# Performance work log

Hardware: AMD Instinct MI355X
Metric: run time of the kernel (lower is better)

The kernel has to match this reference:

```python
import jax, jax.numpy as jnp
import numpy as np
import math

# dims
B, L, D = 2, 2048, 1024          # batch, seq len, embedding_dim
HID, ATT, H = 1024, 512, 8       # linear_hidden_dim, attention_dim, num_heads
DQK, DUV = ATT // H, HID // H    # 64, 128
NBUCK = 64                       # time_num_buckets
MAX_SPAN = 86400 * 90            # max_time_span
EPS = 1e-6
OUT_DIM = 2 * HID + 2 * ATT      # uvqk output dim = 3072


def _time_boundaries():
    # RelativeAttentionBiasModule._build_boundaries: pure log buckets
    steps = NBUCK - 1
    log_part = np.exp(np.linspace(0.0, math.log(MAX_SPAN), steps))
    b = np.unique(np.floor(np.clip(log_part, 1, None)).astype(np.int64)).astype(np.float32)
    return jnp.asarray(b)

_BOUNDARIES = _time_boundaries()  # len <= 63, indices < NBUCK


def setup_inputs() -> dict:
    key = jax.random.key(0)
    ks = jax.random.split(key, 8)
    x = jax.random.normal(ks[0], (B, L, D), dtype=jnp.float32)
    timestamps = jnp.sort(
        jax.random.randint(ks[1], (B, L), 0, 2592000), axis=-1
    )  # chronological event times (seconds)
    attn_mask = jnp.tril(jnp.ones((L, L), dtype=bool))[None].repeat(B, axis=0)  # causal
    W_uvqk = jax.random.normal(ks[2], (OUT_DIM, D), dtype=jnp.float32) * 0.02
    b_uvqk = jnp.zeros((OUT_DIM,), dtype=jnp.float32)
    time_bias = jax.random.normal(ks[3], (NBUCK, H), dtype=jnp.float32) * 0.02
    W_o = jax.random.normal(ks[4], (D, HID), dtype=jnp.float32) * 0.02
    b_o = jnp.zeros((D,), dtype=jnp.float32)
    rms_w = jnp.ones((HID,), dtype=jnp.float32)
    return {"x": x, "timestamps": timestamps, "attn_mask": attn_mask,
            "W_uvqk": W_uvqk, "b_uvqk": b_uvqk, "time_bias": time_bias,
            "W_o": W_o, "b_o": b_o, "rms_w": rms_w}


def reference(x, timestamps, attn_mask, W_uvqk, b_uvqk, time_bias, W_o, b_o, rms_w):
    Bx, Lx, _ = x.shape
    scale = 1.0 / math.sqrt(DQK)

    # fused uvqk projection + act1 (silu)
    h = jax.nn.silu(x @ W_uvqk.T + b_uvqk)  # [B, L, OUT_DIM]
    u, v, q, k = jnp.split(h, [HID, 2 * HID, 2 * HID + ATT], axis=-1)

    def heads(t, d):  # [B, L, H*d] -> [B, H, L, d]
        return t.reshape(Bx, Lx, H, d).transpose(0, 2, 1, 3)

    u = heads(u, DUV)
    v = heads(v, DUV)
    q = heads(q, DQK) * scale
    k = heads(k, DQK)

    logits = jnp.einsum('bhid,bhjd->bhij', q.astype(jnp.float32), k.astype(jnp.float32))

    # bucketized relative-time bias (per-head)
    tdiff = jnp.abs(timestamps[:, :, None] - timestamps[:, None, :])
    tdiff = jnp.clip(tdiff, 1, None).astype(jnp.float32)  # clamp_min(1)
    bk = jnp.searchsorted(_BOUNDARIES, tdiff, side='left')  # torch.bucketize right=False
    rab = time_bias[bk].transpose(0, 3, 1, 2)  # [B, H, L, L]

    # pointwise silu attention (no softmax), masked
    A = jax.nn.silu(logits + rab) * attn_mask[:, None].astype(jnp.float32)

    y = jnp.einsum('bhij,bhjd->bhid', A, v)               # [B, H, L, DUV]
    y = y.transpose(0, 2, 1, 3).reshape(Bx, Lx, HID)       # merge heads
    u_m = u.transpose(0, 2, 1, 3).reshape(Bx, Lx, HID)

    # RMSNorm then U-gate
    rms = y * jax.lax.rsqrt(jnp.mean(y * y, axis=-1, keepdims=True) + EPS) * rms_w
    y_point = rms.astype(x.dtype) * u_m

    return y_point @ W_o.T + b_o  # [B, L, D]
```

## Files before the change

### kernel.cpp

```cpp
#include <hip/hip_runtime.h>
#include <hip/hip_bf16.h>

typedef float f32x4 __attribute__((ext_vector_type(4)));
typedef short s16x8 __attribute__((ext_vector_type(8)));
typedef short s16x4 __attribute__((ext_vector_type(4)));
typedef unsigned short u16x4 __attribute__((ext_vector_type(4)));

__device__ __forceinline__ float bf2f(unsigned short u) {
    union { unsigned int i; float f; } x; x.i = ((unsigned int)u) << 16; return x.f;
}
__device__ __forceinline__ unsigned short f2bf(float f) {
    union { float f; unsigned int i; } x; x.f = f;
    unsigned int r = x.i + 0x7FFFu + ((x.i >> 16) & 1u);
    return (unsigned short)(r >> 16);
}
__device__ __forceinline__ float silu(float v) {
    return v / (1.f + __expf(-v));
}
__device__ __forceinline__ float silu_fast(float v) {
    return v * __builtin_amdgcn_rcpf(1.f + __expf(-v));
}

#define GLDS16(gp, lp) __builtin_amdgcn_global_load_lds( \
    (const __attribute__((address_space(1))) unsigned int*)(gp), \
    (__attribute__((address_space(3))) unsigned int*)(lp), 16, 0, 0)

__global__ __launch_bounds__(256) void cvt_bf16(
    const float* __restrict__ X, const float* __restrict__ W,
    const float* __restrict__ Wo,
    unsigned short* __restrict__ Xb, unsigned short* __restrict__ Wb,
    unsigned short* __restrict__ Wob)
{
    int idx = blockIdx.x * 256 + threadIdx.x;
    const float* src; unsigned short* dst; int off;
    if (idx < 1048576)       { src = X;  dst = Xb;  off = idx; }
    else if (idx < 1835008)  { src = W;  dst = Wb;  off = idx - 1048576; }
    else                     { src = Wo; dst = Wob; off = idx - 1835008; }
    f32x4 v = *reinterpret_cast<const f32x4*>(&src[(size_t)off * 4]);
    u16x4 o;
    #pragma unroll
    for (int j = 0; j < 4; ++j) o[j] = f2bf(v[j]);
    *reinterpret_cast<u16x4*>(&dst[(size_t)off * 4]) = o;
}

__global__ __launch_bounds__(256) void bucketize(
    const int* __restrict__ TS, unsigned char* __restrict__ BK)
{
    const int jt = blockIdx.x, it = blockIdx.y, b = blockIdx.z;
    if (jt > it) return;
    __shared__ int bndRaw[63];
    __shared__ int bnd[64];
    __shared__ int tsi[64], tsj[64];
    const int tid = threadIdx.x;
    if (tid < 63) {
        double step = log(7776000.0) / 62.0;
        double v = exp(step * (double)tid);
        if (v < 1.0) v = 1.0;
        bndRaw[tid] = (int)floor(v);
    }
    if (tid >= 64 && tid < 128) tsi[tid - 64] = TS[b * 2048 + it * 64 + (tid - 64)];
    else if (tid >= 128 && tid < 192) tsj[tid - 128] = TS[b * 2048 + jt * 64 + (tid - 128)];
    __syncthreads();
    if (tid == 0) {
        int c = 0, p = -1;
        for (int i = 0; i < 63; ++i) { int x = bndRaw[i]; if (x != p) { bnd[c++] = x; p = x; } }
        for (; c < 64; ++c) bnd[c] = 0x7FFFFFFF;
    }
    __syncthreads();
    const int il = tid & 63, jc = (tid >> 6) * 16;
    const int tiv = tsi[il];
    unsigned char out[16];
    #pragma unroll
    for (int u = 0; u < 16; ++u) {
        int td = tiv - tsj[jc + u]; td = td < 0 ? -td : td; if (td < 1) td = 1;
        int pos = 0;
        #pragma unroll
        for (int st = 32; st; st >>= 1)
            if (bnd[pos + st - 1] < td) pos += st;
        out[u] = (unsigned char)pos;
    }
    *reinterpret_cast<int4*>(&BK[((size_t)b << 22) + (size_t)(it * 64 + il) * 2048 + jt * 64 + jc]) =
        *reinterpret_cast<const int4*>(out);
}

__global__ __launch_bounds__(256) void gemm_uvqk(
    const unsigned short* __restrict__ Xb, const unsigned short* __restrict__ Wb,
    const float* __restrict__ bias,
    unsigned short* __restrict__ U, unsigned short* __restrict__ Vt,
    unsigned short* __restrict__ Q, unsigned short* __restrict__ K)
{
    __shared__ unsigned short sA[128][32];
    __shared__ unsigned short sB[128][32];
    const int tid = threadIdx.x;
    const int wv = tid >> 6, lane = tid & 63;
    const int g = lane >> 4, lr = lane & 15;
    const int wid = (blockIdx.x & 7) * 96 + (blockIdx.x >> 3);
    const int m0 = (wid & 31) * 128, n0 = (wid >> 5) * 128;
    const int wr = (wv >> 1) * 64, wc = (wv & 1) * 64;
    const int srow = (lane >> 2), scol = (lane & 3) * 8;
    f32x4 acc[4][4] = {};

    for (int k0 = 0; k0 < 1024; k0 += 32) {
        #pragma unroll
        for (int c = 0; c < 2; ++c) {
            int rb = (wv * 2 + c) * 16;
            GLDS16(&Xb[(size_t)(m0 + rb + srow) * 1024 + k0 + scol], &sA[rb][0]);
            GLDS16(&Wb[(size_t)(n0 + rb + srow) * 1024 + k0 + scol], &sB[rb][0]);
        }
        __syncthreads();
        s16x8 afr[4], bfr[4];
        #pragma unroll
        for (int i = 0; i < 4; ++i)
            afr[i] = *reinterpret_cast<const s16x8*>(&sA[wr + i * 16 + lr][g * 8]);
        #pragma unroll
        for (int i = 0; i < 4; ++i)
            bfr[i] = *reinterpret_cast<const s16x8*>(&sB[wc + i * 16 + lr][g * 8]);
        #pragma unroll
        for (int mi = 0; mi < 4; ++mi)
            #pragma unroll
            for (int ni = 0; ni < 4; ++ni)
                acc[mi][ni] = __builtin_amdgcn_mfma_f32_16x16x32_bf16(
                    afr[mi], bfr[ni], acc[mi][ni], 0, 0, 0);
        __syncthreads();
    }

    #pragma unroll
    for (int ni = 0; ni < 4; ++ni) {
        int n = n0 + wc + ni * 16 + lr;
        float bn = bias[n];
        #pragma unroll
        for (int mi = 0; mi < 4; ++mi) {
            #pragma unroll
            for (int r = 0; r < 4; ++r) {
                int m = m0 + wr + mi * 16 + g * 4 + r;
                float v = silu(acc[mi][ni][r] + bn);
                int b = m >> 11, l = m & 2047;
                if (n < 1024) {
                    U[(size_t)m * 1024 + n] = f2bf(v);
                } else if (n < 2048) {
                    int dd = n - 1024, h = dd >> 7, d = dd & 127;
                    Vt[(((size_t)(b * 8 + h) * 128 + d) << 11) + l] = f2bf(v);
                } else if (n < 2560) {
                    int dd = n - 2048, h = dd >> 6, d = dd & 63;
                    Q[((((size_t)(b * 8 + h) << 11) + l) << 6) + d] = f2bf(v * 0.125f);
                } else {
                    int dd = n - 2560, h = dd >> 6, d = dd & 63;
                    K[((((size_t)(b * 8 + h) << 11) + l) << 6) + d] = f2bf(v);
                }
            }
        }
    }
}

__global__ __launch_bounds__(512, 1) void attn(
    const unsigned short* __restrict__ Q, const unsigned short* __restrict__ K,
    const unsigned short* __restrict__ Vt, const unsigned char* __restrict__ BK,
    const float* __restrict__ TB, float* __restrict__ Y)
{
    __shared__ __align__(16) unsigned short sK[2][2][64][64];
    __shared__ __align__(16) unsigned short sV[2][2][128][64];
    __shared__ __align__(16) unsigned char  sBK[2][2][64][64];

    const int tid = threadIdx.x, wv = tid >> 6, lane = tid & 63;
    const int g = lane >> 4, lr = lane & 15;

    const int bid = blockIdx.x;
    const int xcd = bid & 7, kix = bid >> 3;
    const int bh = 2 * xcd + (kix & 1);
    const int ti = 31 - (kix >> 1);
    const int b = bh >> 3, h = bh & 7;
    const int i0 = ti * 64;
    const int rg = wv & 3;
    const int half = wv >> 2;
    const int irow = i0 + rg * 16;
    const int P = (ti + 2) >> 1;

    const int tbl = __float_as_int(TB[lane * 8 + h]);

    const unsigned short* qb = Q + ((size_t)bh << 11) * 64;
    const unsigned short* kb = K + ((size_t)bh << 11) * 64;
    const unsigned short* vtb = Vt + ((size_t)bh << 7) * 2048;
    const unsigned char* bkb = BK + ((size_t)b << 22);

    s16x8 aq[2];
    #pragma unroll
    for (int kq = 0; kq < 2; ++kq)
        aq[kq] = *reinterpret_cast<const s16x8*>(&qb[(size_t)(irow + lr) * 64 + kq * 32 + g * 8]);

    char* sKb = (char*)&sK[0][0][0][0];
    char* sVb = (char*)&sV[0][0][0][0];
    char* sBKb = (char*)&sBK[0][0][0][0];
    const int cs = lr & 7;
    const int ib = irow + lr;

    auto stage = [&](int q, int db) {
        int jth = 2 * q + half;
        if (jth > ti) jth = 2 * q;
        const size_t j0 = (size_t)jth * 64;
        char* kd = sKb + db * 16384 + half * 8192;
        char* vd = sVb + db * 32768 + half * 16384;
        char* bkd = sBKb + db * 8192 + half * 4096;
        #pragma unroll
        for (int c = 0; c < 2; ++c) {
            int chunk = rg * 128 + c * 64 + lane;
            int row = chunk >> 3, c8 = chunk & 7;
            GLDS16(kb + (j0 + row) * 64 + ((c8 ^ (row & 7)) * 8), kd + chunk * 16);
        }
        #pragma unroll
        for (int c = 0; c < 4; ++c) {
            int chunk = rg * 256 + c * 64 + lane;
            int d = chunk >> 3, c8 = chunk & 7;
            GLDS16(vtb + (size_t)d * 2048 + j0 + ((c8 ^ (d & 7)) * 8), vd + chunk * 16);
        }
        {
            int chunk = rg * 64 + lane;
            int row = chunk >> 2, c16 = chunk & 3;
            GLDS16(bkb + (size_t)(i0 + row) * 2048 + j0 + ((c16 ^ (row & 3)) * 16), bkd + chunk * 16);
        }
    };

    f32x4 accy[8] = {};

#define COMPUTE(DB) { \
        const int jt = 2 * p + half; \
        if (jt <= ti) { \
            const char* kbase = sKb + (DB) * 16384 + half * 8192; \
            f32x4 sacc[4] = {}; \
            _Pragma("unroll") \
            for (int ni = 0; ni < 4; ++ni) { \
                _Pragma("unroll") \
                for (int kq = 0; kq < 2; ++kq) { \
                    s16x8 kf = *reinterpret_cast<const s16x8*>( \
                        kbase + (ni * 16 + lr) * 128 + (((kq * 4 + g) ^ cs) << 4)); \
                    sacc[ni] = __builtin_amdgcn_mfma_f32_16x16x32_bf16(kf, aq[kq], sacc[ni], 0, 0, 0); \
                } \
            } \
            const int j0 = jt * 64; \
            const bool diag = (jt == ti); \
            s16x4 pf[4]; \
            _Pragma("unroll") \
            for (int ni = 0; ni < 4; ++ni) { \
                unsigned int bw = *reinterpret_cast<const unsigned int*>( \
                    sBKb + (DB) * 8192 + half * 4096 + (rg * 16 + lr) * 64 + ((ni ^ (lr & 3)) << 4) + g * 4); \
                float b0 = __int_as_float(__builtin_amdgcn_ds_bpermute((int)((bw & 255u) << 2), tbl)); \
                float b1 = __int_as_float(__builtin_amdgcn_ds_bpermute((int)(((bw >> 8) & 255u) << 2), tbl)); \
                float b2 = __int_as_float(__builtin_amdgcn_ds_bpermute((int)(((bw >> 16) & 255u) << 2), tbl)); \
                float b3 = __int_as_float(__builtin_amdgcn_ds_bpermute((int)((bw >> 24) << 2), tbl)); \
                float v0 = silu_fast(sacc[ni][0] + b0); \
                float v1 = silu_fast(sacc[ni][1] + b1); \
                float v2 = silu_fast(sacc[ni][2] + b2); \
                float v3 = silu_fast(sacc[ni][3] + b3); \
                if (diag) { \
                    int jb = j0 + ni * 16 + g * 4; \
                    if (jb + 0 > ib) v0 = 0.f; \
                    if (jb + 1 > ib) v1 = 0.f; \
                    if (jb + 2 > ib) v2 = 0.f; \
                    if (jb + 3 > ib) v3 = 0.f; \
                } \
                unsigned int w0, w1; \
                asm("v_cvt_pk_bf16_f32 %0, %1, %2" : "=v"(w0) : "v"(v0), "v"(v1)); \
                asm("v_cvt_pk_bf16_f32 %0, %1, %2" : "=v"(w1) : "v"(v2), "v"(v3)); \
                union { unsigned int u_[2]; s16x4 v_; } cvt_; \
                cvt_.u_[0] = w0; cvt_.u_[1] = w1; \
                pf[ni] = cvt_.v_; \
            } \
            const char* vbase = sVb + (DB) * 32768 + half * 16384; \
            _Pragma("unroll") \
            for (int di = 0; di < 8; ++di) { \
                _Pragma("unroll") \
                for (int ni = 0; ni < 4; ++ni) { \
                    s16x4 vf = *reinterpret_cast<const s16x4*>( \
                        vbase + (di * 16 + lr) * 128 + (((2 * ni + (g >> 1)) ^ cs) << 4) + ((g & 1) << 3)); \
                    accy[di] = __builtin_amdgcn_mfma_f32_16x16x16bf16_1k(pf[ni], vf, accy[di], 0, 0, 0); \
                } \
            } \
        } }

    stage(0, 0);

    int p = 0;
    for (;;) {
        __builtin_amdgcn_s_barrier();
        if (p + 1 < P) {
            stage(p + 1, 1);
            asm volatile("s_waitcnt vmcnt(7)" ::: "memory");
        } else {
            asm volatile("s_waitcnt vmcnt(0)" ::: "memory");
        }
        __builtin_amdgcn_s_barrier();
        COMPUTE(0);
        if (++p == P) break;
        __builtin_amdgcn_s_barrier();
        if (p + 1 < P) {
            stage(p + 1, 0);
            asm volatile("s_waitcnt vmcnt(7)" ::: "memory");
        } else {
            asm volatile("s_waitcnt vmcnt(0)" ::: "memory");
        }
        __builtin_amdgcn_s_barrier();
        COMPUTE(1);
        if (++p == P) break;
    }
#undef COMPUTE

    __syncthreads();
    float* red = (float*)sVb;
    if (wv >= 4) {
        #pragma unroll
        for (int di = 0; di < 8; ++di)
            #pragma unroll
            for (int r = 0; r < 4; ++r)
                red[(rg * 16 + g * 4 + r) * 132 + di * 16 + lr] = accy[di][r];
    }
    __syncthreads();
    if (wv < 4) {
        #pragma unroll
        for (int di = 0; di < 8; ++di)
            #pragma unroll
            for (int r = 0; r < 4; ++r) {
                float s = accy[di][r] + red[(rg * 16 + g * 4 + r) * 132 + di * 16 + lr];
                Y[(size_t)((b << 11) + irow + g * 4 + r) * 1024 + h * 128 + di * 16 + lr] = s;
            }
    }
}

__global__ __launch_bounds__(256) void rmsnorm_gate(
    const float* __restrict__ Y, const unsigned short* __restrict__ U,
    const float* __restrict__ rw, unsigned short* __restrict__ YP)
{
    __shared__ float red[4];
    const int row = blockIdx.x, tid = threadIdx.x;
    f32x4 v = *reinterpret_cast<const f32x4*>(&Y[(size_t)row * 1024 + tid * 4]);
    float ss = v[0] * v[0] + v[1] * v[1] + v[2] * v[2] + v[3] * v[3];
    #pragma unroll
    for (int off = 32; off; off >>= 1) ss += __shfl_down(ss, off);
    if ((tid & 63) == 0) red[tid >> 6] = ss;
    __syncthreads();
    float rms = rsqrtf((red[0] + red[1] + red[2] + red[3]) * (1.f / 1024.f) + 1e-6f);
    #pragma unroll
    for (int j = 0; j < 4; ++j) {
        int c = tid * 4 + j;
        float o = v[j] * rms * rw[c] * bf2f(U[(size_t)row * 1024 + c]);
        YP[(size_t)row * 1024 + c] = f2bf(o);
    }
}

__global__ __launch_bounds__(512) void gemm_out(
    const unsigned short* __restrict__ YP, const unsigned short* __restrict__ Wob,
    const float* __restrict__ bo, float* __restrict__ OUT)
{
    __shared__ unsigned short sA[128][32];
    __shared__ unsigned short sB[128][32];
    const int tid = threadIdx.x;
    const int wv = tid >> 6, lane = tid & 63;
    const int g = lane >> 4, lr = lane & 15;
    const int wid = (blockIdx.x & 7) * 32 + (blockIdx.x >> 3);
    const int m0 = (wid & 31) * 128, n0 = (wid >> 5) * 128;
    const int wr = (wv >> 2) * 64, wc = (wv & 3) * 32;
    f32x4 acc[4][2] = {};

    const int srow = tid >> 2, scol = (tid & 3) * 8;

    for (int k0 = 0; k0 < 1024; k0 += 32) {
        GLDS16(&YP[(size_t)(m0 + srow) * 1024 + k0 + scol], &sA[srow][scol]);
        GLDS16(&Wob[(size_t)(n0 + srow) * 1024 + k0 + scol], &sB[srow][scol]);
        __syncthreads();
        s16x8 afr[4], bfr[2];
        #pragma unroll
        for (int i = 0; i < 4; ++i)
            afr[i] = *reinterpret_cast<const s16x8*>(&sA[wr + i * 16 + lr][g * 8]);
        #pragma unroll
        for (int i = 0; i < 2; ++i)
            bfr[i] = *reinterpret_cast<const s16x8*>(&sB[wc + i * 16 + lr][g * 8]);
        #pragma unroll
        for (int mi = 0; mi < 4; ++mi)
            #pragma unroll
            for (int ni = 0; ni < 2; ++ni)
                acc[mi][ni] = __builtin_amdgcn_mfma_f32_16x16x32_bf16(
                    afr[mi], bfr[ni], acc[mi][ni], 0, 0, 0);
        __syncthreads();
    }

    #pragma unroll
    for (int ni = 0; ni < 2; ++ni) {
        int n = n0 + wc + ni * 16 + lr;
        float bn = bo[n];
        #pragma unroll
        for (int mi = 0; mi < 4; ++mi)
            #pragma unroll
            for (int r = 0; r < 4; ++r) {
                int m = m0 + wr + mi * 16 + g * 4 + r;
                OUT[(size_t)m * 1024 + n] = acc[mi][ni][r] + bn;
            }
    }
}

extern "C" void kernel_launch(void* const* d_in, const int* in_sizes, int n_in,
                              void* d_out, int out_size, void* d_ws, size_t ws_size,
                              hipStream_t stream) {
    const float* X     = (const float*)d_in[0];
    const int*   TS    = (const int*)d_in[1];
    const float* Wuvqk = (const float*)d_in[3];
    const float* buvqk = (const float*)d_in[4];
    const float* TB    = (const float*)d_in[5];
    const float* Wo    = (const float*)d_in[6];
    const float* bo    = (const float*)d_in[7];
    const float* rw    = (const float*)d_in[8];
    float* OUT = (float*)d_out;

    char* ws = (char*)d_ws;
    unsigned short* Qb  = (unsigned short*)(ws);
    unsigned short* Kb  = (unsigned short*)(ws + (4u << 20));
    unsigned short* Vt  = (unsigned short*)(ws + (8u << 20));
    unsigned short* Ub  = (unsigned short*)(ws + (16u << 20));
    float*          Yb  = (float*)(ws + (24u << 20));
    unsigned short* Xb  = (unsigned short*)(ws + (24u << 20));
    unsigned short* Wb  = (unsigned short*)(ws + (32u << 20));
    unsigned short* YP  = (unsigned short*)(ws + (40u << 20));
    unsigned char*  BKm = (unsigned char*)(ws + (48u << 20));
    unsigned short* Wob = (unsigned short*)(ws + (56u << 20));

    cvt_bf16<<<8192, 256, 0, stream>>>(X, Wuvqk, Wo, Xb, Wb, Wob);
    bucketize<<<dim3(32, 32, 2), 256, 0, stream>>>(TS, BKm);
    gemm_uvqk<<<768, 256, 0, stream>>>(Xb, Wb, buvqk, Ub, Vt, Qb, Kb);
    attn<<<512, 512, 0, stream>>>(Qb, Kb, Vt, BKm, TB, Yb);
    rmsnorm_gate<<<4096, 256, 0, stream>>>(Yb, Ub, rw, YP);
    gemm_out<<<256, 512, 0, stream>>>(YP, Wob, bo, OUT);
}
```

Before: 149.8 us.

## Double GEMM K-tile to 64 with XOR-swizzled LDS and transposed V stores

```diff
diff --git a/kernel.cpp b/kernel.cpp
--- a/kernel.cpp
+++ b/kernel.cpp
@@ -89,63 +89,96 @@
     unsigned short* __restrict__ U, unsigned short* __restrict__ Vt,
     unsigned short* __restrict__ Q, unsigned short* __restrict__ K)
 {
-    __shared__ unsigned short sA[128][32];
-    __shared__ unsigned short sB[128][32];
+    __shared__ __align__(16) unsigned short smem[2][128][64];
     const int tid = threadIdx.x;
     const int wv = tid >> 6, lane = tid & 63;
     const int g = lane >> 4, lr = lane & 15;
     const int wid = (blockIdx.x & 7) * 96 + (blockIdx.x >> 3);
     const int m0 = (wid & 31) * 128, n0 = (wid >> 5) * 128;
     const int wr = (wv >> 1) * 64, wc = (wv & 1) * 64;
-    const int srow = (lane >> 2), scol = (lane & 3) * 8;
+    const int ls = lr & 7;
     f32x4 acc[4][4] = {};
 
-    for (int k0 = 0; k0 < 1024; k0 += 32) {
-        #pragma unroll
-        for (int c = 0; c < 2; ++c) {
-            int rb = (wv * 2 + c) * 16;
-            GLDS16(&Xb[(size_t)(m0 + rb + srow) * 1024 + k0 + scol], &sA[rb][0]);
-            GLDS16(&Wb[(size_t)(n0 + rb + srow) * 1024 + k0 + scol], &sB[rb][0]);
+    for (int k0 = 0; k0 < 1024; k0 += 64) {
+        #pragma unroll
+        for (int c = 0; c < 4; ++c) {
+            int id = c * 256 + tid;
+            int row = id >> 3, c8 = id & 7;
+            int sc = (c8 ^ (row & 7)) * 8;
+            GLDS16(&Xb[(size_t)(m0 + row) * 1024 + k0 + sc], &smem[0][row][c8 * 8]);
+            GLDS16(&Wb[(size_t)(n0 + row) * 1024 + k0 + sc], &smem[1][row][c8 * 8]);
         }
         __syncthreads();
-        s16x8 afr[4], bfr[4];
+        s16x8 afr[4][2], bfr[4][2];
         #pragma unroll
         for (int i = 0; i < 4; ++i)
-            afr[i] = *reinterpret_cast<const s16x8*>(&sA[wr + i * 16 + lr][g * 8]);
-        #pragma unroll
-        for (int i = 0; i < 4; ++i)
-            bfr[i] = *reinterpret_cast<const s16x8*>(&sB[wc + i * 16 + lr][g * 8]);
-        #pragma unroll
-        for (int mi = 0; mi < 4; ++mi)
-            #pragma unroll
-            for (int ni = 0; ni < 4; ++ni)
-                acc[mi][ni] = __builtin_amdgcn_mfma_f32_16x16x32_bf16(
-                    afr[mi], bfr[ni], acc[mi][ni], 0, 0, 0);
+            #pragma unroll
+            for (int kq = 0; kq < 2; ++kq) {
+                afr[i][kq] = *reinterpret_cast<const s16x8*>(
+                    &smem[0][wr + i * 16 + lr][((kq * 4 + g) ^ ls) * 8]);
+                bfr[i][kq] = *reinterpret_cast<const s16x8*>(
+                    &smem[1][wc + i * 16 + lr][((kq * 4 + g) ^ ls) * 8]);
+            }
+        #pragma unroll
+        for (int kq = 0; kq < 2; ++kq)
+            #pragma unroll
+            for (int mi = 0; mi < 4; ++mi)
+                #pragma unroll
+                for (int ni = 0; ni < 4; ++ni)
+                    acc[mi][ni] = __builtin_amdgcn_mfma_f32_16x16x32_bf16(
+                        afr[mi][kq], bfr[ni][kq], acc[mi][ni], 0, 0, 0);
         __syncthreads();
     }
 
-    #pragma unroll
-    for (int ni = 0; ni < 4; ++ni) {
-        int n = n0 + wc + ni * 16 + lr;
-        float bn = bias[n];
-        #pragma unroll
-        for (int mi = 0; mi < 4; ++mi) {
-            #pragma unroll
-            for (int r = 0; r < 4; ++r) {
-                int m = m0 + wr + mi * 16 + g * 4 + r;
-                float v = silu(acc[mi][ni][r] + bn);
-                int b = m >> 11, l = m & 2047;
-                if (n < 1024) {
-                    U[(size_t)m * 1024 + n] = f2bf(v);
-                } else if (n < 2048) {
-                    int dd = n - 1024, h = dd >> 7, d = dd & 127;
-                    Vt[(((size_t)(b * 8 + h) * 128 + d) << 11) + l] = f2bf(v);
-                } else if (n < 2560) {
-                    int dd = n - 2048, h = dd >> 6, d = dd & 63;
-                    Q[((((size_t)(b * 8 + h) << 11) + l) << 6) + d] = f2bf(v * 0.125f);
-                } else {
-                    int dd = n - 2560, h = dd >> 6, d = dd & 63;
-                    K[((((size_t)(b * 8 + h) << 11) + l) << 6) + d] = f2bf(v);
+    if (n0 >= 1024 && n0 < 2048) {
+        const int head = (n0 - 1024) >> 7;
+        unsigned short* sT = &smem[0][0][0] + wv * (32 * 72);
+        #pragma unroll
+        for (int hh = 0; hh < 2; ++hh) {
+            #pragma unroll
+            for (int nn = 0; nn < 2; ++nn) {
+                int ni = hh * 2 + nn;
+                float bn = bias[n0 + wc + ni * 16 + lr];
+                #pragma unroll
+                for (int mi = 0; mi < 4; ++mi)
+                    #pragma unroll
+                    for (int r = 0; r < 4; ++r)
+                        sT[(nn * 16 + lr) * 72 + mi * 16 + g * 4 + r] =
+                            f2bf(silu(acc[mi][ni][r] + bn));
+            }
+            #pragma unroll
+            for (int c = 0; c < 4; ++c) {
+                int id = c * 64 + lane;
+                int row = id >> 3, ch = id & 7;
+                s16x8 val = *reinterpret_cast<const s16x8*>(&sT[row * 72 + ch * 8]);
+                int d = wc + hh * 32 + row;
+                int mg = m0 + wr + ch * 8;
+                int bb = mg >> 11, l = mg & 2047;
+                *reinterpret_cast<s16x8*>(
+                    &Vt[(((size_t)(bb * 8 + head) * 128 + d) << 11) + l]) = val;
+            }
+        }
+    } else {
+        #pragma unroll
+        for (int ni = 0; ni < 4; ++ni) {
+            int n = n0 + wc + ni * 16 + lr;
+            float bn = bias[n];
+            #pragma unroll
+            for (int mi = 0; mi < 4; ++mi) {
+                #pragma unroll
+                for (int r = 0; r < 4; ++r) {
+                    int m = m0 + wr + mi * 16 + g * 4 + r;
+                    float v = silu(acc[mi][ni][r] + bn);
+                    int b = m >> 11, l = m & 2047;
+                    if (n < 1024) {
+                        U[(size_t)m * 1024 + n] = f2bf(v);
+                    } else if (n < 2560) {
+                        int dd = n - 2048, h = dd >> 6, d = dd & 63;
+                        Q[((((size_t)(b * 8 + h) << 11) + l) << 6) + d] = f2bf(v * 0.125f);
+                    } else {
+                        int dd = n - 2560, h = dd >> 6, d = dd & 63;
+                        K[((((size_t)(b * 8 + h) << 11) + l) << 6) + d] = f2bf(v);
+                    }
                 }
             }
         }
@@ -349,35 +382,47 @@
     const unsigned short* __restrict__ YP, const unsigned short* __restrict__ Wob,
     const float* __restrict__ bo, float* __restrict__ OUT)
 {
-    __shared__ unsigned short sA[128][32];
-    __shared__ unsigned short sB[128][32];
+    __shared__ __align__(16) unsigned short sA[128][64];
+    __shared__ __align__(16) unsigned short sB[128][64];
     const int tid = threadIdx.x;
     const int wv = tid >> 6, lane = tid & 63;
     const int g = lane >> 4, lr = lane & 15;
     const int wid = (blockIdx.x & 7) * 32 + (blockIdx.x >> 3);
     const int m0 = (wid & 31) * 128, n0 = (wid >> 5) * 128;
     const int wr = (wv >> 2) * 64, wc = (wv & 3) * 32;
+    const int ls = lr & 7;
     f32x4 acc[4][2] = {};
 
-    const int srow = tid >> 2, scol = (tid & 3) * 8;
-
-    for (int k0 = 0; k0 < 1024; k0 += 32) {
-        GLDS16(&YP[(size_t)(m0 + srow) * 1024 + k0 + scol], &sA[srow][scol]);
-        GLDS16(&Wob[(size_t)(n0 + srow) * 1024 + k0 + scol], &sB[srow][scol]);
+    for (int k0 = 0; k0 < 1024; k0 += 64) {
+        #pragma unroll
+        for (int c = 0; c < 2; ++c) {
+            int id = c * 512 + tid;
+            int row = id >> 3, c8 = id & 7;
+            int sc = (c8 ^ (row & 7)) * 8;
+            GLDS16(&YP[(size_t)(m0 + row) * 1024 + k0 + sc], &sA[row][c8 * 8]);
+            GLDS16(&Wob[(size_t)(n0 + row) * 1024 + k0 + sc], &sB[row][c8 * 8]);
+        }
         __syncthreads();
-        s16x8 afr[4], bfr[2];
-        #pragma unroll
-        for (int i = 0; i < 4; ++i)
-            afr[i] = *reinterpret_cast<const s16x8*>(&sA[wr + i * 16 + lr][g * 8]);
-        #pragma unroll
-        for (int i = 0; i < 2; ++i)
-            bfr[i] = *reinterpret_cast<const s16x8*>(&sB[wc + i * 16 + lr][g * 8]);
-        #pragma unroll
-        for (int mi = 0; mi < 4; ++mi)
-            #pragma unroll
-            for (int ni = 0; ni < 2; ++ni)
-                acc[mi][ni] = __builtin_amdgcn_mfma_f32_16x16x32_bf16(
-                    afr[mi], bfr[ni], acc[mi][ni], 0, 0, 0);
+        s16x8 afr[4][2], bfr[2][2];
+        #pragma unroll
+        for (int kq = 0; kq < 2; ++kq) {
+            #pragma unroll
+            for (int i = 0; i < 4; ++i)
+                afr[i][kq] = *reinterpret_cast<const s16x8*>(
+                    &sA[wr + i * 16 + lr][((kq * 4 + g) ^ ls) * 8]);
+            #pragma unroll
+            for (int i = 0; i < 2; ++i)
+                bfr[i][kq] = *reinterpret_cast<const s16x8*>(
+                    &sB[wc + i * 16 + lr][((kq * 4 + g) ^ ls) * 8]);
+        }
+        #pragma unroll
+        for (int kq = 0; kq < 2; ++kq)
+            #pragma unroll
+            for (int mi = 0; mi < 4; ++mi)
+                #pragma unroll
+                for (int ni = 0; ni < 2; ++ni)
+                    acc[mi][ni] = __builtin_amdgcn_mfma_f32_16x16x32_bf16(
+                        afr[mi][kq], bfr[ni][kq], acc[mi][ni], 0, 0, 0);
         __syncthreads();
     }
 
```

New measurement: 149.7 us. Within noise of the previous version (-0.1%).

## Multi-stage async LDS pipeline and larger tiles for projection GEMMs

Applied to the files above, without the earlier changes.

```diff
diff --git a/kernel.cpp b/kernel.cpp
--- a/kernel.cpp
+++ b/kernel.cpp
@@ -83,45 +83,62 @@
         *reinterpret_cast<const int4*>(out);
 }
 
-__global__ __launch_bounds__(256) void gemm_uvqk(
+__global__ __launch_bounds__(512, 2) void gemm_uvqk(
     const unsigned short* __restrict__ Xb, const unsigned short* __restrict__ Wb,
     const float* __restrict__ bias,
     unsigned short* __restrict__ U, unsigned short* __restrict__ Vt,
     unsigned short* __restrict__ Q, unsigned short* __restrict__ K)
 {
-    __shared__ unsigned short sA[128][32];
-    __shared__ unsigned short sB[128][32];
+    __shared__ __align__(16) unsigned short sA[4][256][32];
+    __shared__ __align__(16) unsigned short sB[4][256][32];
     const int tid = threadIdx.x;
     const int wv = tid >> 6, lane = tid & 63;
     const int g = lane >> 4, lr = lane & 15;
-    const int wid = (blockIdx.x & 7) * 96 + (blockIdx.x >> 3);
-    const int m0 = (wid & 31) * 128, n0 = (wid >> 5) * 128;
-    const int wr = (wv >> 1) * 64, wc = (wv & 1) * 64;
-    const int srow = (lane >> 2), scol = (lane & 3) * 8;
-    f32x4 acc[4][4] = {};
-
-    for (int k0 = 0; k0 < 1024; k0 += 32) {
+    const int wid = (blockIdx.x & 7) * 24 + (blockIdx.x >> 3);
+    const int mt = wid & 15, nt = wid >> 4;
+    const int m0 = mt * 256, n0 = nt * 256;
+    const int wr = (wv >> 2) * 128, wc = (wv & 3) * 64;
+    f32x4 acc[8][4] = {};
+
+    auto stage = [&](int kt) {
+        const int db = kt & 3;
+        const int k0 = kt * 32;
         #pragma unroll
         for (int c = 0; c < 2; ++c) {
-            int rb = (wv * 2 + c) * 16;
-            GLDS16(&Xb[(size_t)(m0 + rb + srow) * 1024 + k0 + scol], &sA[rb][0]);
-            GLDS16(&Wb[(size_t)(n0 + rb + srow) * 1024 + k0 + scol], &sB[rb][0]);
-        }
-        __syncthreads();
-        s16x8 afr[4], bfr[4];
+            int idx = c * 512 + tid;
+            int row = idx >> 2, co = (idx & 3) * 8;
+            GLDS16(&Xb[(size_t)(m0 + row) * 1024 + k0 + co], &sA[db][row][co]);
+            GLDS16(&Wb[(size_t)(n0 + row) * 1024 + k0 + co], &sB[db][row][co]);
+        }
+    };
+
+    stage(0); stage(1); stage(2);
+    for (int kt = 0; kt < 32; ++kt) {
+        const int db = kt & 3;
+        __builtin_amdgcn_s_barrier();
+        if (kt < 29) {
+            stage(kt + 3);
+            asm volatile("s_waitcnt vmcnt(12)" ::: "memory");
+        } else if (kt == 29) {
+            asm volatile("s_waitcnt vmcnt(8)" ::: "memory");
+        } else if (kt == 30) {
+            asm volatile("s_waitcnt vmcnt(4)" ::: "memory");
+        } else {
+            asm volatile("s_waitcnt vmcnt(0)" ::: "memory");
+        }
+        __builtin_amdgcn_s_barrier();
+        s16x8 bfr[4];
         #pragma unroll
         for (int i = 0; i < 4; ++i)
-            afr[i] = *reinterpret_cast<const s16x8*>(&sA[wr + i * 16 + lr][g * 8]);
-        #pragma unroll
-        for (int i = 0; i < 4; ++i)
-            bfr[i] = *reinterpret_cast<const s16x8*>(&sB[wc + i * 16 + lr][g * 8]);
-        #pragma unroll
-        for (int mi = 0; mi < 4; ++mi)
+            bfr[i] = *reinterpret_cast<const s16x8*>(&sB[db][wc + i * 16 + lr][g * 8]);
+        #pragma unroll
+        for (int mi = 0; mi < 8; ++mi) {
+            s16x8 af = *reinterpret_cast<const s16x8*>(&sA[db][wr + mi * 16 + lr][g * 8]);
             #pragma unroll
             for (int ni = 0; ni < 4; ++ni)
                 acc[mi][ni] = __builtin_amdgcn_mfma_f32_16x16x32_bf16(
-                    afr[mi], bfr[ni], acc[mi][ni], 0, 0, 0);
-        __syncthreads();
+                    af, bfr[ni], acc[mi][ni], 0, 0, 0);
+        }
     }
 
     #pragma unroll
@@ -129,11 +146,11 @@
         int n = n0 + wc + ni * 16 + lr;
         float bn = bias[n];
         #pragma unroll
-        for (int mi = 0; mi < 4; ++mi) {
+        for (int mi = 0; mi < 8; ++mi) {
             #pragma unroll
             for (int r = 0; r < 4; ++r) {
                 int m = m0 + wr + mi * 16 + g * 4 + r;
-                float v = silu(acc[mi][ni][r] + bn);
+                float v = silu_fast(acc[mi][ni][r] + bn);
                 int b = m >> 11, l = m & 2047;
                 if (n < 1024) {
                     U[(size_t)m * 1024 + n] = f2bf(v);
@@ -345,12 +362,12 @@
     }
 }
 
-__global__ __launch_bounds__(512) void gemm_out(
+__global__ __launch_bounds__(512, 2) void gemm_out(
     const unsigned short* __restrict__ YP, const unsigned short* __restrict__ Wob,
     const float* __restrict__ bo, float* __restrict__ OUT)
 {
-    __shared__ unsigned short sA[128][32];
-    __shared__ unsigned short sB[128][32];
+    __shared__ __align__(16) unsigned short sA[4][128][32];
+    __shared__ __align__(16) unsigned short sB[4][128][32];
     const int tid = threadIdx.x;
     const int wv = tid >> 6, lane = tid & 63;
     const int g = lane >> 4, lr = lane & 15;
@@ -359,26 +376,42 @@
     const int wr = (wv >> 2) * 64, wc = (wv & 3) * 32;
     f32x4 acc[4][2] = {};
 
-    const int srow = tid >> 2, scol = (tid & 3) * 8;
-
-    for (int k0 = 0; k0 < 1024; k0 += 32) {
-        GLDS16(&YP[(size_t)(m0 + srow) * 1024 + k0 + scol], &sA[srow][scol]);
-        GLDS16(&Wob[(size_t)(n0 + srow) * 1024 + k0 + scol], &sB[srow][scol]);
-        __syncthreads();
-        s16x8 afr[4], bfr[2];
-        #pragma unroll
-        for (int i = 0; i < 4; ++i)
-            afr[i] = *reinterpret_cast<const s16x8*>(&sA[wr + i * 16 + lr][g * 8]);
+    const int srow = tid >> 2, sc8 = (tid & 3) * 8;
+
+    auto stage = [&](int kt) {
+        const int db = kt & 3;
+        const int k0 = kt * 32;
+        GLDS16(&YP[(size_t)(m0 + srow) * 1024 + k0 + sc8], &sA[db][srow][sc8]);
+        GLDS16(&Wob[(size_t)(n0 + srow) * 1024 + k0 + sc8], &sB[db][srow][sc8]);
+    };
+
+    stage(0); stage(1); stage(2);
+    for (int kt = 0; kt < 32; ++kt) {
+        const int db = kt & 3;
+        __builtin_amdgcn_s_barrier();
+        if (kt < 29) {
+            stage(kt + 3);
+            asm volatile("s_waitcnt vmcnt(6)" ::: "memory");
+        } else if (kt == 29) {
+            asm volatile("s_waitcnt vmcnt(4)" ::: "memory");
+        } else if (kt == 30) {
+            asm volatile("s_waitcnt vmcnt(2)" ::: "memory");
+        } else {
+            asm volatile("s_waitcnt vmcnt(0)" ::: "memory");
+        }
+        __builtin_amdgcn_s_barrier();
+        s16x8 bfr[2];
         #pragma unroll
         for (int i = 0; i < 2; ++i)
-            bfr[i] = *reinterpret_cast<const s16x8*>(&sB[wc + i * 16 + lr][g * 8]);
-        #pragma unroll
-        for (int mi = 0; mi < 4; ++mi)
+            bfr[i] = *reinterpret_cast<const s16x8*>(&sB[db][wc + i * 16 + lr][g * 8]);
+        #pragma unroll
+        for (int mi = 0; mi < 4; ++mi) {
+            s16x8 af = *reinterpret_cast<const s16x8*>(&sA[db][wr + mi * 16 + lr][g * 8]);
             #pragma unroll
             for (int ni = 0; ni < 2; ++ni)
                 acc[mi][ni] = __builtin_amdgcn_mfma_f32_16x16x32_bf16(
-                    afr[mi], bfr[ni], acc[mi][ni], 0, 0, 0);
-        __syncthreads();
+                    af, bfr[ni], acc[mi][ni], 0, 0, 0);
+        }
     }
 
     #pragma unroll
@@ -422,7 +455,7 @@
 
     cvt_bf16<<<8192, 256, 0, stream>>>(X, Wuvqk, Wo, Xb, Wb, Wob);
     bucketize<<<dim3(32, 32, 2), 256, 0, stream>>>(TS, BKm);
-    gemm_uvqk<<<768, 256, 0, stream>>>(Xb, Wb, buvqk, Ub, Vt, Qb, Kb);
+    gemm_uvqk<<<192, 512, 0, stream>>>(Xb, Wb, buvqk, Ub, Vt, Qb, Kb);
     attn<<<512, 512, 0, stream>>>(Qb, Kb, Vt, BKm, TB, Yb);
     rmsnorm_gate<<<4096, 256, 0, stream>>>(Yb, Ub, rw, YP);
     gemm_out<<<256, 512, 0, stream>>>(YP, Wob, bo, OUT);
```

Result: slower. 168.9 us (+12.8%).
